# Kernel tuning notes

Measured on AMD Instinct MI355X. Metric: run time of the kernel, lower is better.

## Reference

```python
import jax, jax.numpy as jnp
import numpy as np

N, S, H = 100000, 150, 150
G = 4  # gates: input, output, forget, update


def setup_inputs() -> dict:
    key = jax.random.key(0)
    ks = jax.random.split(key, 10)
    scale = 1.0 / np.sqrt(H)
    return {
        "s_in": jax.random.normal(ks[0], (N, S), jnp.float32),
        "s_out": jax.random.normal(ks[1], (N, S), jnp.float32),
        "h_in": jax.random.normal(ks[2], (N, H), jnp.float32),
        "h_out": jax.random.normal(ks[3], (N, H), jnp.float32),
        "last_c": jax.random.normal(ks[4], (N, H), jnp.float32),
        "w_in": jax.random.normal(ks[5], (G, S, H), jnp.float32) * scale,
        "w_out": jax.random.normal(ks[6], (G, S, H), jnp.float32) * scale,
        "u_in": jax.random.normal(ks[7], (G, H, H), jnp.float32) * scale,
        "u_out": jax.random.normal(ks[8], (G, H, H), jnp.float32) * scale,
        "b": jax.random.normal(ks[9], (G, H), jnp.float32) * scale,
    }


def reference(s_in, s_out, h_in, h_out, last_c, w_in, w_out, u_in, u_out, b):
    # gates[g] = sigmoid(s_in @ w_in[g] + s_out @ w_out[g] + h_in @ u_in[g]
    #                    + h_out @ u_out[g] + b[g])   -> shape [G, N, H]
    pre = (jnp.einsum("ns,gsh->gnh", s_in, w_in)
           + jnp.einsum("ns,gsh->gnh", s_out, w_out)
           + jnp.einsum("nh,ghk->gnk", h_in, u_in)
           + jnp.einsum("nh,ghk->gnk", h_out, u_out)
           + b[:, None, :])
    gates = jax.nn.sigmoid(pre)
    input_gate, output_gate, forget_gate, update_gate = gates
    cell_state = forget_gate * last_c + update_gate * input_gate
    hidden_state = output_gate * jnp.tanh(cell_state)
    return hidden_state, cell_state
```

## Files before the change

kernel.cpp:

```cpp
#include <hip/hip_runtime.h>
#include <stdint.h>

#define NROWS 100000
#define SDIM 150
#define HDIM 150
#define KSEG 160
#define NKB 20
#define NCOL 640
#define BM 128
#define NTHREADS 512
#define BSLICE 40960
#define ASLICE 8192
#define BUFBYTES (BSLICE + ASLICE)
#define EPI_STRIDE 656

using half8  = __attribute__((ext_vector_type(8))) _Float16;
using half2v = __attribute__((ext_vector_type(2))) _Float16;
using floatx4 = __attribute__((ext_vector_type(4))) float;

__device__ __forceinline__ float fsig(float x) {
  return __builtin_amdgcn_rcpf(1.0f + __expf(-x));
}
__device__ __forceinline__ float ftanh(float x) {
  return 2.0f * __builtin_amdgcn_rcpf(1.0f + __expf(-2.0f * x)) - 1.0f;
}

__device__ __forceinline__ void gload_lds16(const void* g, void* l) {
  __builtin_amdgcn_global_load_lds(
      (const __attribute__((address_space(1))) void*)g,
      (__attribute__((address_space(3))) void*)l, 16, 0, 0);
}

#define KBAR(VM)                                              \
  do {                                                        \
    asm volatile("s_waitcnt vmcnt(" #VM ")" ::: "memory");    \
    asm volatile("s_waitcnt lgkmcnt(0)" ::: "memory");        \
    __builtin_amdgcn_s_barrier();                             \
    asm volatile("" ::: "memory");                            \
  } while (0)

__global__ void pack_w_kernel(const float* __restrict__ w_in,
                              const float* __restrict__ w_out,
                              const float* __restrict__ u_in,
                              const float* __restrict__ u_out,
                              _Float16* __restrict__ wblk) {
  int idx = blockIdx.x * 256 + threadIdx.x;
  if (idx >= NKB * NCOL * 32) return;
  int j    = idx & 7;
  int slot = (idx >> 3) & 3;
  int col  = (idx >> 5) % NCOL;
  int kb   = idx / (NCOL * 32);
  int kg   = slot ^ ((col >> 1) & 3);
  int k    = kb * 32 + kg * 8 + j;
  int seg  = k / KSEG;
  int kl   = k - seg * KSEG;
  int g    = col / KSEG;
  int h    = col - g * KSEG;
  float v = 0.0f;
  if (kl < SDIM && h < HDIM) {
    const float* src = (seg == 0) ? w_in : (seg == 1) ? w_out
                     : (seg == 2) ? u_in : u_out;
    v = src[(g * SDIM + kl) * HDIM + h];
  }
  wblk[idx] = (_Float16)v;
}

__global__ __launch_bounds__(NTHREADS, 2) void lstm_fused_kernel(
    const float* __restrict__ s_in, const float* __restrict__ s_out,
    const float* __restrict__ h_in, const float* __restrict__ h_out,
    const float* __restrict__ last_c, const float* __restrict__ bias,
    const _Float16* __restrict__ wblk,
    float* __restrict__ out_hid, float* __restrict__ out_cell) {
  __shared__ __align__(16) char lds[3 * BUFBYTES];

  const int tid  = threadIdx.x;
  const int lane = tid & 63;
  const int l15  = lane & 15;
  const int kgrp = lane >> 4;
  const int wid  = tid >> 6;
  const int gate = wid >> 1;
  const int cb   = wid * 80;
  const int row0 = blockIdx.x * BM;

  const float* segp[4] = {s_in, s_out, h_in, h_out};

  floatx4 acc[8][5] = {};

  float bfrag[5];
#pragma unroll
  for (int n = 0; n < 5; ++n) {
    int h = (wid & 1) * 80 + n * 16 + l15;
    bfrag[n] = (h < HDIM) ? bias[gate * HDIM + h] : 0.f;
  }

  const int a_row = tid >> 2;
  const int a_q   = tid & 3;
  const long n_a  = (long)row0 + a_row;
  const bool a_ok = (n_a < NROWS);
  const int a_off = a_row * 64 + ((a_q ^ ((a_row >> 1) & 3)) * 16);

  char* buf0 = lds;
  char* buf1 = lds + BUFBYTES;
  char* buf2 = lds + 2 * BUFBYTES;

  auto stageB = [&](int kb, char* buf) {
    const char* g = (const char*)wblk + (size_t)kb * BSLICE + tid * 16;
    char* d = buf + tid * 16;
#pragma unroll
    for (int i = 0; i < 5; ++i)
      gload_lds16(g + i * 8192, d + i * 8192);
  };
  auto loadA = [&](int kb, float4& lo, float4& hi) {
    lo = make_float4(0.f, 0.f, 0.f, 0.f);
    hi = make_float4(0.f, 0.f, 0.f, 0.f);
    const int seg = kb / 5;
    const int kls = (kb % 5) * 32 + a_q * 8;
    if (a_ok && kls < SDIM) {
      const float* p = segp[seg] + (size_t)n_a * SDIM + kls;
      if (kls + 7 < SDIM) {
        lo = *(const float4*)p;
        hi = *(const float4*)(p + 4);
      } else {
        float t[8] = {0.f, 0.f, 0.f, 0.f, 0.f, 0.f, 0.f, 0.f};
#pragma unroll
        for (int i = 0; i < 8; ++i)
          if (kls + i < SDIM) t[i] = p[i];
        lo = make_float4(t[0], t[1], t[2], t[3]);
        hi = make_float4(t[4], t[5], t[6], t[7]);
      }
    }
  };
  auto commitA = [&](char* buf, float4 lo, float4 hi) {
    union { _Float16 h[8]; uint4 u; } pk;
    pk.h[0] = (_Float16)lo.x; pk.h[1] = (_Float16)lo.y;
    pk.h[2] = (_Float16)lo.z; pk.h[3] = (_Float16)lo.w;
    pk.h[4] = (_Float16)hi.x; pk.h[5] = (_Float16)hi.y;
    pk.h[6] = (_Float16)hi.z; pk.h[7] = (_Float16)hi.w;
    *(uint4*)(buf + BSLICE + a_off) = pk.u;
  };
  auto compute = [&](const char* bufc) {
    const char* aB = bufc + BSLICE;
    half8 bf[5];
#pragma unroll
    for (int n = 0; n < 5; ++n) {
      int col = cb + n * 16 + l15;
      bf[n] = *(const half8*)(bufc + col * 64 + ((kgrp ^ ((col >> 1) & 3)) * 16));
    }
#pragma unroll
    for (int mt = 0; mt < 8; ++mt) {
      int r = mt * 16 + l15;
      half8 af = *(const half8*)(aB + r * 64 + ((kgrp ^ ((r >> 1) & 3)) * 16));
#pragma unroll
      for (int n = 0; n < 5; ++n)
        acc[mt][n] = __builtin_amdgcn_mfma_f32_16x16x32_f16(af, bf[n], acc[mt][n], 0, 0, 0);
    }
  };

  float4 anl, anh;
  {
    float4 a0l, a0h;
    stageB(0, buf0); loadA(0, a0l, a0h);
    stageB(1, buf1); loadA(1, anl, anh);
    commitA(buf0, a0l, a0h);
    KBAR(7);
  }

  char* bc = buf0;
  char* bn = buf1;
  char* bs = buf2;
#pragma unroll 1
  for (int t = 0; t < NKB; ++t) {
    float4 avl, avh;
    const bool has2 = (t + 2 < NKB);
    if (has2) {
      stageB(t + 2, bs);
      loadA(t + 2, avl, avh);
    }
    if (t + 1 < NKB) commitA(bn, anl, anh);
    compute(bc);
    anl = avl; anh = avh;
    if (has2) KBAR(7); else KBAR(0);
    char* tmp = bc; bc = bn; bn = bs; bs = tmp;
  }

  _Float16* epi = (_Float16*)lds;
#pragma unroll
  for (int s = 0; s < 4; ++s) {
    if (s) __syncthreads();
#pragma unroll
    for (int mt2 = 0; mt2 < 2; ++mt2) {
      const int mt = 2 * s + mt2;
#pragma unroll
      for (int n = 0; n < 5; ++n) {
        int col = cb + n * 16 + l15;
#pragma unroll
        for (int i = 0; i < 4; ++i) {
          int rl = mt2 * 16 + kgrp * 4 + i;
          float gv = fsig(acc[mt][n][i] + bfrag[n]);
          epi[rl * EPI_STRIDE + col] = (_Float16)gv;
        }
      }
    }
    __syncthreads();
#pragma unroll
    for (int it = 0; it < 5; ++it) {
      int idx = tid + it * NTHREADS;
      if (idx < 32 * 75) {
        int row = idx / 75;
        int h2  = idx - row * 75;
        long n = (long)row0 + s * 32 + row;
        if (n < NROWS) {
          int h = h2 * 2;
          const _Float16* er = epi + row * EPI_STRIDE + h;
          half2v gi = *(const half2v*)(er + 0 * 160);
          half2v go = *(const half2v*)(er + 1 * 160);
          half2v gf = *(const half2v*)(er + 2 * 160);
          half2v gu = *(const half2v*)(er + 3 * 160);
          float2 lc = *(const float2*)(last_c + n * HDIM + h);
          float c0 = (float)gf[0] * lc.x + (float)gu[0] * (float)gi[0];
          float c1 = (float)gf[1] * lc.y + (float)gu[1] * (float)gi[1];
          float hd0 = (float)go[0] * ftanh(c0);
          float hd1 = (float)go[1] * ftanh(c1);
          *(float2*)(out_hid  + n * HDIM + h) = make_float2(hd0, hd1);
          *(float2*)(out_cell + n * HDIM + h) = make_float2(c0, c1);
        }
      }
    }
  }
}

extern "C" void kernel_launch(void* const* d_in, const int* in_sizes, int n_in,
                              void* d_out, int out_size, void* d_ws, size_t ws_size,
                              hipStream_t stream) {
  const float* s_in   = (const float*)d_in[0];
  const float* s_out  = (const float*)d_in[1];
  const float* h_in   = (const float*)d_in[2];
  const float* h_out  = (const float*)d_in[3];
  const float* last_c = (const float*)d_in[4];
  const float* w_in   = (const float*)d_in[5];
  const float* w_out  = (const float*)d_in[6];
  const float* u_in   = (const float*)d_in[7];
  const float* u_out  = (const float*)d_in[8];
  const float* b      = (const float*)d_in[9];

  _Float16* wblk = (_Float16*)d_ws;

  pack_w_kernel<<<(NKB * NCOL * 32 + 255) / 256, 256, 0, stream>>>(
      w_in, w_out, u_in, u_out, wblk);

  float* out_hid  = (float*)d_out;
  float* out_cell = out_hid + (size_t)NROWS * HDIM;

  lstm_fused_kernel<<<(NROWS + BM - 1) / BM, NTHREADS, 0, stream>>>(
      s_in, s_out, h_in, h_out, last_c, b, wblk, out_hid, out_cell);
}
```

Baseline: 251.5 us.

## Replace direct-to-LDS triple buffering with register-staged double buffering

The weight-slice staging changes from global_load_lds into a three-buffer LDS ring to ordinary global loads into registers, which are written to a two-buffer LDS ring one iteration later. A-tile prefetch runs two stages ahead using two alternating register sets, with the loop unrolled by two. MFMA sections get raised wave priority through s_setprio. The smaller LDS footprint is meant to allow more resident blocks and drop the vmcnt waits, but it costs extra VGPRs, and the min-occupancy hint in launch_bounds is removed.

```diff
diff --git a/kernel.cpp b/kernel.cpp
--- a/kernel.cpp
+++ b/kernel.cpp
@@ -25,15 +25,8 @@
   return 2.0f * __builtin_amdgcn_rcpf(1.0f + __expf(-2.0f * x)) - 1.0f;
 }
 
-__device__ __forceinline__ void gload_lds16(const void* g, void* l) {
-  __builtin_amdgcn_global_load_lds(
-      (const __attribute__((address_space(1))) void*)g,
-      (__attribute__((address_space(3))) void*)l, 16, 0, 0);
-}
-
-#define KBAR(VM)                                              \
+#define LBAR()                                                \
   do {                                                        \
-    asm volatile("s_waitcnt vmcnt(" #VM ")" ::: "memory");    \
     asm volatile("s_waitcnt lgkmcnt(0)" ::: "memory");        \
     __builtin_amdgcn_s_barrier();                             \
     asm volatile("" ::: "memory");                            \
@@ -65,13 +58,13 @@
   wblk[idx] = (_Float16)v;
 }
 
-__global__ __launch_bounds__(NTHREADS, 2) void lstm_fused_kernel(
+__global__ __launch_bounds__(NTHREADS) void lstm_fused_kernel(
     const float* __restrict__ s_in, const float* __restrict__ s_out,
     const float* __restrict__ h_in, const float* __restrict__ h_out,
     const float* __restrict__ last_c, const float* __restrict__ bias,
     const _Float16* __restrict__ wblk,
     float* __restrict__ out_hid, float* __restrict__ out_cell) {
-  __shared__ __align__(16) char lds[3 * BUFBYTES];
+  __shared__ __align__(16) char lds[2 * BUFBYTES];
 
   const int tid  = threadIdx.x;
   const int lane = tid & 63;
@@ -99,16 +92,19 @@
   const bool a_ok = (n_a < NROWS);
   const int a_off = a_row * 64 + ((a_q ^ ((a_row >> 1) & 3)) * 16);
 
-  char* buf0 = lds;
-  char* buf1 = lds + BUFBYTES;
-  char* buf2 = lds + 2 * BUFBYTES;
-
-  auto stageB = [&](int kb, char* buf) {
+  char* cur = lds;
+  char* nxt = lds + BUFBYTES;
+
+  uint4 bR0, bR1, bR2, bR3, bR4;
+  float4 aE_lo, aE_hi, aO_lo, aO_hi;
+
+  auto loadB = [&](int kb) {
     const char* g = (const char*)wblk + (size_t)kb * BSLICE + tid * 16;
-    char* d = buf + tid * 16;
-#pragma unroll
-    for (int i = 0; i < 5; ++i)
-      gload_lds16(g + i * 8192, d + i * 8192);
+    bR0 = *(const uint4*)(g);
+    bR1 = *(const uint4*)(g + 8192);
+    bR2 = *(const uint4*)(g + 16384);
+    bR3 = *(const uint4*)(g + 24576);
+    bR4 = *(const uint4*)(g + 32768);
   };
   auto loadA = [&](int kb, float4& lo, float4& hi) {
     lo = make_float4(0.f, 0.f, 0.f, 0.f);
@@ -130,7 +126,15 @@
       }
     }
   };
-  auto commitA = [&](char* buf, float4 lo, float4 hi) {
+  auto writeB = [&](char* buf) {
+    char* d = buf + tid * 16;
+    *(uint4*)(d)         = bR0;
+    *(uint4*)(d + 8192)  = bR1;
+    *(uint4*)(d + 16384) = bR2;
+    *(uint4*)(d + 24576) = bR3;
+    *(uint4*)(d + 32768) = bR4;
+  };
+  auto commitA = [&](char* buf, const float4& lo, const float4& hi) {
     union { _Float16 h[8]; uint4 u; } pk;
     pk.h[0] = (_Float16)lo.x; pk.h[1] = (_Float16)lo.y;
     pk.h[2] = (_Float16)lo.z; pk.h[3] = (_Float16)lo.w;
@@ -146,6 +150,7 @@
       int col = cb + n * 16 + l15;
       bf[n] = *(const half8*)(bufc + col * 64 + ((kgrp ^ ((col >> 1) & 3)) * 16));
     }
+    __builtin_amdgcn_s_setprio(1);
 #pragma unroll
     for (int mt = 0; mt < 8; ++mt) {
       int r = mt * 16 + l15;
@@ -154,33 +159,33 @@
       for (int n = 0; n < 5; ++n)
         acc[mt][n] = __builtin_amdgcn_mfma_f32_16x16x32_f16(af, bf[n], acc[mt][n], 0, 0, 0);
     }
-  };
-
-  float4 anl, anh;
-  {
-    float4 a0l, a0h;
-    stageB(0, buf0); loadA(0, a0l, a0h);
-    stageB(1, buf1); loadA(1, anl, anh);
-    commitA(buf0, a0l, a0h);
-    KBAR(7);
-  }
-
-  char* bc = buf0;
-  char* bn = buf1;
-  char* bs = buf2;
+    __builtin_amdgcn_s_setprio(0);
+  };
+
+  loadA(0, aE_lo, aE_hi);
+  loadA(1, aO_lo, aO_hi);
+  loadB(0);
+  writeB(cur);
+  commitA(cur, aE_lo, aE_hi);
+  loadA(2, aE_lo, aE_hi);
+  loadB(1);
+  LBAR();
+
+  auto body = [&](int t, float4& pubLo, float4& pubHi) {
+    if (t + 1 < NKB) {
+      writeB(nxt);
+      commitA(nxt, pubLo, pubHi);
+    }
+    if (t + 2 < NKB) loadB(t + 2);
+    if (t + 3 < NKB) loadA(t + 3, pubLo, pubHi);
+    compute(cur);
+    LBAR();
+    char* tmp = cur; cur = nxt; nxt = tmp;
+  };
 #pragma unroll 1
-  for (int t = 0; t < NKB; ++t) {
-    float4 avl, avh;
-    const bool has2 = (t + 2 < NKB);
-    if (has2) {
-      stageB(t + 2, bs);
-      loadA(t + 2, avl, avh);
-    }
-    if (t + 1 < NKB) commitA(bn, anl, anh);
-    compute(bc);
-    anl = avl; anh = avh;
-    if (has2) KBAR(7); else KBAR(0);
-    char* tmp = bc; bc = bn; bn = bs; bs = tmp;
+  for (int t = 0; t < NKB; t += 2) {
+    body(t,     aO_lo, aO_hi);
+    body(t + 1, aE_lo, aE_hi);
   }
 
   _Float16* epi = (_Float16*)lds;
```

New measurement: 222.9 us. 11.4% less time.

## Split columns across two blocks, interleave gate columns, single-buffer LDS

Applied to the files above, without the earlier changes.

Packs weights so the four gates of each hidden unit sit in adjacent columns, which lets each block own half the hidden units (320 columns) and a 64-row tile. The kernel now uses 256 threads with a single LDS stage instead of triple buffering, aiming for higher occupancy (4 blocks per CU). The epilogue reads all four gates with one 16-byte load. MFMA sections are wrapped in s_setprio. The trade-off is that the A input rows are now read by two blocks each, and load/compute overlap is weaker because every step waits on vmcnt(0).

```diff
diff --git a/kernel.cpp b/kernel.cpp
--- a/kernel.cpp
+++ b/kernel.cpp
@@ -4,18 +4,17 @@
 #define NROWS 100000
 #define SDIM 150
 #define HDIM 150
-#define KSEG 160
 #define NKB 20
-#define NCOL 640
-#define BM 128
-#define NTHREADS 512
-#define BSLICE 40960
-#define ASLICE 8192
-#define BUFBYTES (BSLICE + ASLICE)
-#define EPI_STRIDE 656
+#define NCOLF 640
+#define BN 320
+#define BM 64
+#define NTHREADS 256
+#define BSLICE_FULL 40960
+#define BSTAGE 20480
+#define ASTAGE 4096
+#define EPIW 328
 
 using half8  = __attribute__((ext_vector_type(8))) _Float16;
-using half2v = __attribute__((ext_vector_type(2))) _Float16;
 using floatx4 = __attribute__((ext_vector_type(4))) float;
 
 __device__ __forceinline__ float fsig(float x) {
@@ -31,9 +30,16 @@
       (__attribute__((address_space(3))) void*)l, 16, 0, 0);
 }
 
-#define KBAR(VM)                                              \
+#define BAR_FULL()                                            \
   do {                                                        \
-    asm volatile("s_waitcnt vmcnt(" #VM ")" ::: "memory");    \
+    asm volatile("s_waitcnt vmcnt(0)" ::: "memory");          \
+    asm volatile("s_waitcnt lgkmcnt(0)" ::: "memory");        \
+    __builtin_amdgcn_s_barrier();                             \
+    asm volatile("" ::: "memory");                            \
+  } while (0)
+
+#define BAR_LDS()                                             \
+  do {                                                        \
     asm volatile("s_waitcnt lgkmcnt(0)" ::: "memory");        \
     __builtin_amdgcn_s_barrier();                             \
     asm volatile("" ::: "memory");                            \
@@ -45,17 +51,17 @@
                               const float* __restrict__ u_out,
                               _Float16* __restrict__ wblk) {
   int idx = blockIdx.x * 256 + threadIdx.x;
-  if (idx >= NKB * NCOL * 32) return;
+  if (idx >= NKB * NCOLF * 32) return;
   int j    = idx & 7;
   int slot = (idx >> 3) & 3;
-  int col  = (idx >> 5) % NCOL;
-  int kb   = idx / (NCOL * 32);
+  int col  = (idx >> 5) % NCOLF;
+  int kb   = idx / (NCOLF * 32);
   int kg   = slot ^ ((col >> 1) & 3);
   int k    = kb * 32 + kg * 8 + j;
-  int seg  = k / KSEG;
-  int kl   = k - seg * KSEG;
-  int g    = col / KSEG;
-  int h    = col - g * KSEG;
+  int seg  = k / 160;
+  int kl   = k - seg * 160;
+  int g    = col & 3;
+  int h    = col >> 2;
   float v = 0.0f;
   if (kl < SDIM && h < HDIM) {
     const float* src = (seg == 0) ? w_in : (seg == 1) ? w_out
@@ -65,32 +71,35 @@
   wblk[idx] = (_Float16)v;
 }
 
-__global__ __launch_bounds__(NTHREADS, 2) void lstm_fused_kernel(
+__global__ __launch_bounds__(NTHREADS, 4) void lstm_fused_kernel(
     const float* __restrict__ s_in, const float* __restrict__ s_out,
     const float* __restrict__ h_in, const float* __restrict__ h_out,
     const float* __restrict__ last_c, const float* __restrict__ bias,
     const _Float16* __restrict__ wblk,
     float* __restrict__ out_hid, float* __restrict__ out_cell) {
-  __shared__ __align__(16) char lds[3 * BUFBYTES];
+  __shared__ __align__(16) char lds[BSTAGE + ASTAGE];
 
   const int tid  = threadIdx.x;
   const int lane = tid & 63;
   const int l15  = lane & 15;
   const int kgrp = lane >> 4;
-  const int wid  = tid >> 6;
-  const int gate = wid >> 1;
-  const int cb   = wid * 80;
-  const int row0 = blockIdx.x * BM;
+  const int cgrp = tid >> 6;
+  const int rb   = blockIdx.x >> 1;
+  const int cblk = blockIdx.x & 1;
+  const int cb0  = cblk * BN;
+  const int h0   = cblk * 80;
+  const int row0 = rb * BM;
 
   const float* segp[4] = {s_in, s_out, h_in, h_out};
 
-  floatx4 acc[8][5] = {};
+  floatx4 acc[4][5] = {};
 
   float bfrag[5];
 #pragma unroll
   for (int n = 0; n < 5; ++n) {
-    int h = (wid & 1) * 80 + n * 16 + l15;
-    bfrag[n] = (h < HDIM) ? bias[gate * HDIM + h] : 0.f;
+    int col = cb0 + cgrp * 80 + n * 16 + l15;
+    int h = col >> 2, g = col & 3;
+    bfrag[n] = (h < HDIM) ? bias[g * HDIM + h] : 0.f;
   }
 
   const int a_row = tid >> 2;
@@ -99,105 +108,91 @@
   const bool a_ok = (n_a < NROWS);
   const int a_off = a_row * 64 + ((a_q ^ ((a_row >> 1) & 3)) * 16);
 
-  char* buf0 = lds;
-  char* buf1 = lds + BUFBYTES;
-  char* buf2 = lds + 2 * BUFBYTES;
-
-  auto stageB = [&](int kb, char* buf) {
-    const char* g = (const char*)wblk + (size_t)kb * BSLICE + tid * 16;
-    char* d = buf + tid * 16;
-#pragma unroll
-    for (int i = 0; i < 5; ++i)
-      gload_lds16(g + i * 8192, d + i * 8192);
-  };
-  auto loadA = [&](int kb, float4& lo, float4& hi) {
-    lo = make_float4(0.f, 0.f, 0.f, 0.f);
-    hi = make_float4(0.f, 0.f, 0.f, 0.f);
+  char* ldsB = lds;
+  char* ldsA = lds + BSTAGE;
+
+  float4 rAlo, rAhi;
+
+  auto loadA = [&](int kb) {
+    rAlo = make_float4(0.f, 0.f, 0.f, 0.f);
+    rAhi = make_float4(0.f, 0.f, 0.f, 0.f);
     const int seg = kb / 5;
     const int kls = (kb % 5) * 32 + a_q * 8;
     if (a_ok && kls < SDIM) {
       const float* p = segp[seg] + (size_t)n_a * SDIM + kls;
       if (kls + 7 < SDIM) {
-        lo = *(const float4*)p;
-        hi = *(const float4*)(p + 4);
+        rAlo = *(const float4*)p;
+        rAhi = *(const float4*)(p + 4);
       } else {
         float t[8] = {0.f, 0.f, 0.f, 0.f, 0.f, 0.f, 0.f, 0.f};
 #pragma unroll
         for (int i = 0; i < 8; ++i)
           if (kls + i < SDIM) t[i] = p[i];
-        lo = make_float4(t[0], t[1], t[2], t[3]);
-        hi = make_float4(t[4], t[5], t[6], t[7]);
+        rAlo = make_float4(t[0], t[1], t[2], t[3]);
+        rAhi = make_float4(t[4], t[5], t[6], t[7]);
       }
     }
   };
-  auto commitA = [&](char* buf, float4 lo, float4 hi) {
+  auto commitA = [&]() {
     union { _Float16 h[8]; uint4 u; } pk;
-    pk.h[0] = (_Float16)lo.x; pk.h[1] = (_Float16)lo.y;
-    pk.h[2] = (_Float16)lo.z; pk.h[3] = (_Float16)lo.w;
-    pk.h[4] = (_Float16)hi.x; pk.h[5] = (_Float16)hi.y;
-    pk.h[6] = (_Float16)hi.z; pk.h[7] = (_Float16)hi.w;
-    *(uint4*)(buf + BSLICE + a_off) = pk.u;
-  };
-  auto compute = [&](const char* bufc) {
-    const char* aB = bufc + BSLICE;
+    pk.h[0] = (_Float16)rAlo.x; pk.h[1] = (_Float16)rAlo.y;
+    pk.h[2] = (_Float16)rAlo.z; pk.h[3] = (_Float16)rAlo.w;
+    pk.h[4] = (_Float16)rAhi.x; pk.h[5] = (_Float16)rAhi.y;
+    pk.h[6] = (_Float16)rAhi.z; pk.h[7] = (_Float16)rAhi.w;
+    *(uint4*)(ldsA + a_off) = pk.u;
+  };
+  auto stageB = [&](int kb) {
+    const char* g = (const char*)wblk + (size_t)kb * BSLICE_FULL + cb0 * 64 + tid * 16;
+    char* d = ldsB + tid * 16;
+#pragma unroll
+    for (int i = 0; i < 5; ++i)
+      gload_lds16(g + i * 4096, d + i * 4096);
+  };
+  auto compute = [&]() {
     half8 bf[5];
 #pragma unroll
     for (int n = 0; n < 5; ++n) {
-      int col = cb + n * 16 + l15;
-      bf[n] = *(const half8*)(bufc + col * 64 + ((kgrp ^ ((col >> 1) & 3)) * 16));
-    }
-#pragma unroll
-    for (int mt = 0; mt < 8; ++mt) {
+      int cl = cgrp * 80 + n * 16 + l15;
+      bf[n] = *(const half8*)(ldsB + cl * 64 + ((kgrp ^ ((cl >> 1) & 3)) * 16));
+    }
+    __builtin_amdgcn_s_setprio(1);
+#pragma unroll
+    for (int mt = 0; mt < 4; ++mt) {
       int r = mt * 16 + l15;
-      half8 af = *(const half8*)(aB + r * 64 + ((kgrp ^ ((r >> 1) & 3)) * 16));
+      half8 af = *(const half8*)(ldsA + r * 64 + ((kgrp ^ ((r >> 1) & 3)) * 16));
 #pragma unroll
       for (int n = 0; n < 5; ++n)
         acc[mt][n] = __builtin_amdgcn_mfma_f32_16x16x32_f16(af, bf[n], acc[mt][n], 0, 0, 0);
     }
-  };
-
-  float4 anl, anh;
-  {
-    float4 a0l, a0h;
-    stageB(0, buf0); loadA(0, a0l, a0h);
-    stageB(1, buf1); loadA(1, anl, anh);
-    commitA(buf0, a0l, a0h);
-    KBAR(7);
-  }
-
-  char* bc = buf0;
-  char* bn = buf1;
-  char* bs = buf2;
+    __builtin_amdgcn_s_setprio(0);
+  };
+
+  loadA(0);
 #pragma unroll 1
   for (int t = 0; t < NKB; ++t) {
-    float4 avl, avh;
-    const bool has2 = (t + 2 < NKB);
-    if (has2) {
-      stageB(t + 2, bs);
-      loadA(t + 2, avl, avh);
-    }
-    if (t + 1 < NKB) commitA(bn, anl, anh);
-    compute(bc);
-    anl = avl; anh = avh;
-    if (has2) KBAR(7); else KBAR(0);
-    char* tmp = bc; bc = bn; bn = bs; bs = tmp;
+    stageB(t);
+    commitA();
+    BAR_FULL();
+    if (t + 1 < NKB) loadA(t + 1);
+    compute();
+    BAR_LDS();
   }
 
   _Float16* epi = (_Float16*)lds;
 #pragma unroll
-  for (int s = 0; s < 4; ++s) {
-    if (s) __syncthreads();
+  for (int hh = 0; hh < 2; ++hh) {
+    __syncthreads();
 #pragma unroll
     for (int mt2 = 0; mt2 < 2; ++mt2) {
-      const int mt = 2 * s + mt2;
+      const int mt = hh * 2 + mt2;
 #pragma unroll
       for (int n = 0; n < 5; ++n) {
-        int col = cb + n * 16 + l15;
+        int cl = cgrp * 80 + n * 16 + l15;
 #pragma unroll
         for (int i = 0; i < 4; ++i) {
           int rl = mt2 * 16 + kgrp * 4 + i;
           float gv = fsig(acc[mt][n][i] + bfrag[n]);
-          epi[rl * EPI_STRIDE + col] = (_Float16)gv;
+          epi[rl * EPIW + cl] = (_Float16)gv;
         }
       }
     }
@@ -205,25 +200,20 @@
 #pragma unroll
     for (int it = 0; it < 5; ++it) {
       int idx = tid + it * NTHREADS;
-      if (idx < 32 * 75) {
-        int row = idx / 75;
-        int h2  = idx - row * 75;
-        long n = (long)row0 + s * 32 + row;
-        if (n < NROWS) {
-          int h = h2 * 2;
-          const _Float16* er = epi + row * EPI_STRIDE + h;
-          half2v gi = *(const half2v*)(er + 0 * 160);
-          half2v go = *(const half2v*)(er + 1 * 160);
-          half2v gf = *(const half2v*)(er + 2 * 160);
-          half2v gu = *(const half2v*)(er + 3 * 160);
-          float2 lc = *(const float2*)(last_c + n * HDIM + h);
-          float c0 = (float)gf[0] * lc.x + (float)gu[0] * (float)gi[0];
-          float c1 = (float)gf[1] * lc.y + (float)gu[1] * (float)gi[1];
-          float hd0 = (float)go[0] * ftanh(c0);
-          float hd1 = (float)go[1] * ftanh(c1);
-          *(float2*)(out_hid  + n * HDIM + h) = make_float2(hd0, hd1);
-          *(float2*)(out_cell + n * HDIM + h) = make_float2(c0, c1);
-        }
+      int row = idx / 40;
+      int pr  = idx - row * 40;
+      long n = (long)row0 + hh * 32 + row;
+      int hg = h0 + pr * 2;
+      if (n < NROWS && hg < HDIM) {
+        union { uint4 u; _Float16 f[8]; } gg;
+        gg.u = *(const uint4*)(epi + row * EPIW + pr * 8);
+        float2 lc = *(const float2*)(last_c + (size_t)n * HDIM + hg);
+        float c0 = (float)gg.f[2] * lc.x + (float)gg.f[3] * (float)gg.f[0];
+        float c1 = (float)gg.f[6] * lc.y + (float)gg.f[7] * (float)gg.f[4];
+        float hd0 = (float)gg.f[1] * ftanh(c0);
+        float hd1 = (float)gg.f[5] * ftanh(c1);
+        *(float2*)(out_hid  + (size_t)n * HDIM + hg) = make_float2(hd0, hd1);
+        *(float2*)(out_cell + (size_t)n * HDIM + hg) = make_float2(c0, c1);
       }
     }
   }
@@ -245,12 +235,13 @@
 
   _Float16* wblk = (_Float16*)d_ws;
 
-  pack_w_kernel<<<(NKB * NCOL * 32 + 255) / 256, 256, 0, stream>>>(
+  pack_w_kernel<<<(NKB * NCOLF * 32 + 255) / 256, 256, 0, stream>>>(
       w_in, w_out, u_in, u_out, wblk);
 
   float* out_hid  = (float*)d_out;
   float* out_cell = out_hid + (size_t)NROWS * HDIM;
 
-  lstm_fused_kernel<<<(NROWS + BM - 1) / BM, NTHREADS, 0, stream>>>(
+  const int nrb = (NROWS + BM - 1) / BM;
+  lstm_fused_kernel<<<nrb * 2, NTHREADS, 0, stream>>>(
       s_in, s_out, h_in, h_out, last_c, b, wblk, out_hid, out_cell);
 }
```

Result: faster. 222.8 us (-11.4%).
